# Optimization experiments

Hardware: AMD Instinct MI355X
Metric: run time of the kernel (lower is better)

The kernel has to match this reference:

```python
import jax, jax.numpy as jnp
import numpy as np

B, T, C = 2, 2048, 1024
NH = 16
HD = C // NH  # 64
FF = 4 * C
EPS = 1e-5


def layer_norm(x, w, b):
    mu = jnp.mean(x, axis=-1, keepdims=True)
    var = jnp.mean(jnp.square(x - mu), axis=-1, keepdims=True)
    return (x - mu) * jax.lax.rsqrt(var + EPS) * w + b


def setup_inputs() -> dict:
    key = jax.random.key(0)
    ks = jax.random.split(key, 12)
    s_in = 1.0 / np.sqrt(C)
    s_ff = 1.0 / np.sqrt(FF)
    return {
        "x": jax.random.normal(ks[0], (B, T, C), jnp.float32),
        "ln1_w": jnp.ones((C,), jnp.float32),
        "ln1_b": jnp.zeros((C,), jnp.float32),
        "Wq": jax.random.normal(ks[1], (C, C), jnp.float32) * s_in,
        "Wk": jax.random.normal(ks[2], (C, C), jnp.float32) * s_in,
        "Wv": jax.random.normal(ks[3], (C, C), jnp.float32) * s_in,
        "Wp": jax.random.normal(ks[4], (C, C), jnp.float32) * s_in,
        "bp": jnp.zeros((C,), jnp.float32),
        "ln2_w": jnp.ones((C,), jnp.float32),
        "ln2_b": jnp.zeros((C,), jnp.float32),
        "W1": jax.random.normal(ks[5], (C, FF), jnp.float32) * s_in,
        "b1": jnp.zeros((FF,), jnp.float32),
        "W2": jax.random.normal(ks[6], (FF, C), jnp.float32) * s_ff,
        "b2": jnp.zeros((C,), jnp.float32),
    }


def reference(x, ln1_w, ln1_b, Wq, Wk, Wv, Wp, bp, ln2_w, ln2_b, W1, b1, W2, b2):
    scale = HD ** (-0.5)
    h = layer_norm(x, ln1_w, ln1_b)  # [B,T,C]
    # project and split heads: [B,T,NH,HD] -> [B,NH,T,HD]
    q = (h @ Wq).reshape(B, T, NH, HD).transpose(0, 2, 1, 3)
    k = (h @ Wk).reshape(B, T, NH, HD).transpose(0, 2, 1, 3)
    v = (h @ Wv).reshape(B, T, NH, HD).transpose(0, 2, 1, 3)
    scores = jnp.einsum("bhqd,bhkd->bhqk", q, k) * scale  # [B,NH,T,T]
    causal = jnp.tril(jnp.ones((T, T), jnp.bool_))
    scores = jnp.where(causal, scores, -jnp.inf)
    attn = jax.nn.softmax(scores, axis=-1)
    o = jnp.einsum("bhqk,bhkd->bhqd", attn, v)  # [B,NH,T,HD]
    o = o.transpose(0, 2, 1, 3).reshape(B, T, C)
    x = x + o @ Wp + bp
    h2 = layer_norm(x, ln2_w, ln2_b)
    x = x + jax.nn.relu(h2 @ W1 + b1) @ W2 + b2
    return x
```

## Files before the change

### kernel.cpp

```cpp
#include <hip/hip_runtime.h>
#include <hip/hip_bf16.h>

using u16 = unsigned short;
typedef short v8s __attribute__((ext_vector_type(8)));
typedef float v4f __attribute__((ext_vector_type(4)));

#define B_ 2
#define T_ 2048
#define C_ 1024
#define NH_ 16
#define HD_ 64
#define FF_ 4096
#define NT (B_*T_)
#define QKVC 3072

__device__ __forceinline__ u16 f2b(float f) {
  union { float f; unsigned int i; } v; v.f = f;
  unsigned int r = (v.i + 0x7FFFu + ((v.i >> 16) & 1u)) >> 16;
  return (u16)r;
}
__device__ __forceinline__ v4f mfma16(v8s a, v8s b, v4f c) {
  return __builtin_amdgcn_mfma_f32_16x16x32_bf16(a, b, c, 0, 0, 0);
}
__device__ __forceinline__ void glds16(const u16* g, u16* l) {
  __builtin_amdgcn_global_load_lds(
      (const __attribute__((address_space(1))) unsigned int*)g,
      (__attribute__((address_space(3))) unsigned int*)l, 16, 0, 0);
}

__global__ __launch_bounds__(256) void wcvt_kernel(const float* __restrict__ W,
    u16* __restrict__ Wt, int K, int N) {
  __shared__ float t[32][33];
  int tx = threadIdx.x & 31, ty = threadIdx.x >> 5;
  int n0 = blockIdx.x * 32, k0 = blockIdx.y * 32;
#pragma unroll
  for (int j = 0; j < 4; ++j)
    t[ty + j * 8][tx] = W[(size_t)(k0 + ty + j * 8) * N + n0 + tx];
  __syncthreads();
#pragma unroll
  for (int j = 0; j < 4; ++j)
    Wt[(size_t)(n0 + ty + j * 8) * K + k0 + tx] = f2b(t[tx][ty + j * 8]);
}

__global__ __launch_bounds__(256) void ln_kernel(const float* __restrict__ x,
    const float* __restrict__ w, const float* __restrict__ b, u16* __restrict__ y) {
  int row = blockIdx.x;
  int tid = threadIdx.x;
  const float* xr = x + (size_t)row * C_;
  float4 f4 = *(const float4*)&xr[tid * 4];
  float f[4] = {f4.x, f4.y, f4.z, f4.w};
  float s1 = 0.f, s2 = 0.f;
#pragma unroll
  for (int i = 0; i < 4; ++i) { s1 += f[i]; s2 += f[i] * f[i]; }
#pragma unroll
  for (int off = 32; off > 0; off >>= 1) {
    s1 += __shfl_down(s1, off);
    s2 += __shfl_down(s2, off);
  }
  __shared__ float red[10];
  int lane = tid & 63, wid = tid >> 6;
  if (lane == 0) { red[wid] = s1; red[4 + wid] = s2; }
  __syncthreads();
  if (tid == 0) {
    float a = red[0] + red[1] + red[2] + red[3];
    float q = red[4] + red[5] + red[6] + red[7];
    float mu = a * (1.f / C_);
    float var = q * (1.f / C_) - mu * mu;
    red[8] = mu; red[9] = rsqrtf(var + 1e-5f);
  }
  __syncthreads();
  float mu = red[8], rs = red[9];
  union { uint2 v; u16 s[4]; } st;
#pragma unroll
  for (int i = 0; i < 4; ++i) {
    int c = tid * 4 + i;
    st.s[i] = f2b((f[i] - mu) * rs * w[c] + b[c]);
  }
  *(uint2*)&y[(size_t)row * C_ + tid * 4] = st.v;
}

__global__ __launch_bounds__(256) void gemm_bt(const u16* __restrict__ X,
    const u16* __restrict__ Wt, const float* __restrict__ bias,
    const float* __restrict__ resf, u16* __restrict__ Yb, float* __restrict__ Yf,
    float* __restrict__ Yfz1, int M, int N, int lda, int ldb, int kspl, int relu) {
  __shared__ __align__(16) u16 As[2][128 * 32];
  __shared__ __align__(16) u16 Bs[2][128 * 32];
  int tid = threadIdx.x, lane = tid & 63, w = tid >> 6;
  int wm = w >> 1, wn = w & 1, quad = lane >> 4, lcol = lane & 15;
  int m0 = blockIdx.y * 128, n0 = blockIdx.x * 128;
  int koff = blockIdx.z * kspl;
  v4f acc[4][4] = {};
  int sr = lane >> 2, sc = lane & 3;
  const u16* gA = X  + (size_t)(m0 + w * 32 + sr) * lda + koff + sc * 8;
  const u16* gB = Wt + (size_t)(n0 + w * 32 + sr) * ldb + koff + sc * 8;
  u16* lA0 = As[0] + (w * 32) * 32;
  u16* lA1 = As[1] + (w * 32) * 32;
  u16* lB0 = Bs[0] + (w * 32) * 32;
  u16* lB1 = Bs[1] + (w * 32) * 32;
  for (int k0 = 0; k0 < kspl; k0 += 64) {
    __syncthreads();
    glds16(gA + k0,                        lA0);
    glds16(gA + k0 + (size_t)16 * lda,     lA0 + 16 * 32);
    glds16(gA + k0 + 32,                   lA1);
    glds16(gA + k0 + 32 + (size_t)16 * lda, lA1 + 16 * 32);
    glds16(gB + k0,                        lB0);
    glds16(gB + k0 + (size_t)16 * ldb,     lB0 + 16 * 32);
    glds16(gB + k0 + 32,                   lB1);
    glds16(gB + k0 + 32 + (size_t)16 * ldb, lB1 + 16 * 32);
    __syncthreads();
#pragma unroll
    for (int kh = 0; kh < 2; ++kh) {
      v8s a[4], b[4];
#pragma unroll
      for (int i = 0; i < 4; ++i) {
        a[i] = *(v8s*)&As[kh][(wm * 64 + i * 16 + lcol) * 32 + quad * 8];
        b[i] = *(v8s*)&Bs[kh][(wn * 64 + i * 16 + lcol) * 32 + quad * 8];
      }
#pragma unroll
      for (int i = 0; i < 4; ++i)
#pragma unroll
        for (int j = 0; j < 4; ++j)
          acc[i][j] = mfma16(a[i], b[j], acc[i][j]);
    }
  }
  float* yf = blockIdx.z ? Yfz1 : Yf;
#pragma unroll
  for (int i = 0; i < 4; ++i) {
    int mb = m0 + wm * 64 + i * 16 + quad * 4;
#pragma unroll
    for (int j = 0; j < 4; ++j) {
      int n = n0 + wn * 64 + j * 16 + lcol;
#pragma unroll
      for (int r = 0; r < 4; ++r) {
        float v = acc[i][j][r];
        if (bias) v += bias[n];
        if (resf) v += resf[(size_t)(mb + r) * N + n];
        if (relu) v = fmaxf(v, 0.f);
        if (Yb) Yb[(size_t)(mb + r) * N + n] = f2b(v);
        else    yf[(size_t)(mb + r) * N + n] = v;
      }
    }
  }
}

__global__ __launch_bounds__(256) void gemm_bt_n64(const u16* __restrict__ X,
    const u16* __restrict__ Wt, const float* __restrict__ bias,
    const float* __restrict__ resf, u16* __restrict__ Yb, float* __restrict__ Yf,
    int M, int N, int K, int relu) {
  __shared__ __align__(16) u16 As[128 * 32];
  __shared__ __align__(16) u16 Bs[64 * 32];
  int tid = threadIdx.x, lane = tid & 63, w = tid >> 6;
  int wm = w >> 1, wn = w & 1, quad = lane >> 4, lcol = lane & 15;
  int m0 = blockIdx.y * 128, n0 = blockIdx.x * 64;
  v4f acc[4][2] = {};
  int sr = lane >> 2, sc = lane & 3;
  const u16* gA = X  + (size_t)(m0 + w * 32 + sr) * K + sc * 8;
  const u16* gB = Wt + (size_t)(n0 + w * 16 + sr) * K + sc * 8;
  u16* lA = As + (w * 32) * 32;
  u16* lB = Bs + (w * 16) * 32;
  for (int k0 = 0; k0 < K; k0 += 32) {
    __syncthreads();
    glds16(gA + k0, lA);
    glds16(gA + k0 + (size_t)16 * K, lA + 16 * 32);
    glds16(gB + k0, lB);
    __syncthreads();
    v8s a[4], b[2];
#pragma unroll
    for (int i = 0; i < 4; ++i)
      a[i] = *(v8s*)&As[(wm * 64 + i * 16 + lcol) * 32 + quad * 8];
#pragma unroll
    for (int j = 0; j < 2; ++j)
      b[j] = *(v8s*)&Bs[(wn * 32 + j * 16 + lcol) * 32 + quad * 8];
#pragma unroll
    for (int i = 0; i < 4; ++i)
#pragma unroll
      for (int j = 0; j < 2; ++j)
        acc[i][j] = mfma16(a[i], b[j], acc[i][j]);
  }
#pragma unroll
  for (int i = 0; i < 4; ++i) {
    int mb = m0 + wm * 64 + i * 16 + quad * 4;
#pragma unroll
    for (int j = 0; j < 2; ++j) {
      int n = n0 + wn * 32 + j * 16 + lcol;
#pragma unroll
      for (int r = 0; r < 4; ++r) {
        float v = acc[i][j][r];
        if (bias) v += bias[n];
        if (resf) v += resf[(size_t)(mb + r) * N + n];
        if (relu) v = fmaxf(v, 0.f);
        if (Yb) Yb[(size_t)(mb + r) * N + n] = f2b(v);
        else    Yf[(size_t)(mb + r) * N + n] = v;
      }
    }
  }
}

__global__ __launch_bounds__(256) void add4_kernel(float* __restrict__ out,
    const float* __restrict__ p0, const float* __restrict__ bias,
    const float* __restrict__ res) {
  size_t e0 = ((size_t)blockIdx.x * 256 + threadIdx.x) * 4;
  int col = (int)(e0 & (C_ - 1));
  float4 o = *(float4*)&out[e0];
  float4 p = *(const float4*)&p0[e0];
  float4 r = *(const float4*)&res[e0];
  float4 bb = *(const float4*)&bias[col];
  o.x += p.x + r.x + bb.x;
  o.y += p.y + r.y + bb.y;
  o.z += p.z + r.z + bb.z;
  o.w += p.w + r.w + bb.w;
  *(float4*)&out[e0] = o;
}

__global__ __launch_bounds__(256) void vt_kernel(const u16* __restrict__ QKV,
    u16* __restrict__ VT) {
  int bh = blockIdx.x, tt = blockIdx.y;
  int b = bh >> 4, h = bh & 15;
  int tid = threadIdx.x;
  __shared__ u16 L[64 * 72];
  int r = tid >> 2, g = tid & 3;
  size_t row = ((size_t)(b * T_ + tt * 64 + r)) * QKVC + 2 * C_ + h * HD_;
  union { uint4 v; u16 s[8]; } a0, a1;
  a0.v = *(const uint4*)&QKV[row + g * 8];
  a1.v = *(const uint4*)&QKV[row + 32 + g * 8];
#pragma unroll
  for (int e = 0; e < 8; ++e) L[(g * 8 + e) * 72 + r] = a0.s[e];
#pragma unroll
  for (int e = 0; e < 8; ++e) L[(32 + g * 8 + e) * 72 + r] = a1.s[e];
  __syncthreads();
  size_t orow = ((size_t)(bh * 64 + r)) * T_ + tt * 64;
  *(uint4*)&VT[orow + g * 8]      = *(uint4*)&L[r * 72 + g * 8];
  *(uint4*)&VT[orow + 32 + g * 8] = *(uint4*)&L[r * 72 + 32 + g * 8];
}

__global__ __launch_bounds__(256) void attn_kernel(const u16* __restrict__ QKV,
    const u16* __restrict__ VT, u16* __restrict__ Ob) {
  int bh = blockIdx.x, y = blockIdx.y;
  int b = bh >> 4, h = bh & 15;
  int tid = threadIdx.x, lane = tid & 63, wid = tid >> 6;
  int quad = lane >> 4, lcol = lane & 15;
  __shared__ __align__(16) u16 Ps[4][32 * 72];
  const float SC = 0.125f * 1.44269504f;
  const float EB = 8.0f * 1.44269504f;
  const u16* kbase = QKV + (size_t)b * T_ * QKVC + C_ + h * HD_;
  const u16* vbase = VT + (size_t)(bh * 64) * T_;
  u16* psw = Ps[wid];

  auto ldk = [&](v8s (&ak)[4][2], int kb) {
#pragma unroll
    for (int cg = 0; cg < 4; ++cg)
#pragma unroll
      for (int kh = 0; kh < 2; ++kh)
        ak[cg][kh] = *(const v8s*)&kbase[(size_t)(kb * 64 + cg * 16 + lcol) * QKVC + kh * 32 + quad * 8];
  };

#pragma unroll
  for (int pi = 0; pi < 2; ++pi) {
    int qt = pi ? (15 - y) : y;
    int qg[2];
    v8s bq[2][2];
#pragma unroll
    for (int j = 0; j < 2; ++j) {
      qg[j] = qt * 128 + wid * 32 + j * 16 + lcol;
#pragma unroll
      for (int kh = 0; kh < 2; ++kh)
        bq[j][kh] = *(const v8s*)&QKV[(size_t)(b * T_ + qg[j]) * QKVC + h * HD_ + kh * 32 + quad * 8];
    }
    float l_i[2] = {0.f, 0.f};
    v4f accO[4][2] = {};
    int kbmax = 2 * qt + (wid >> 1);

    auto ctile = [&](v8s (&ak)[4][2], int kb, bool diag) {
      v8s av[4][2];
#pragma unroll
      for (int df = 0; df < 4; ++df)
#pragma unroll
        for (int kh = 0; kh < 2; ++kh)
          av[df][kh] = *(const v8s*)&vbase[(size_t)(df * 16 + lcol) * T_ + kb * 64 + kh * 32 + quad * 8];
#pragma unroll
      for (int j = 0; j < 2; ++j) {
        v4f s[4];
#pragma unroll
        for (int cg = 0; cg < 4; ++cg) {
          v4f acc = {};
          acc = mfma16(ak[cg][1], bq[j][1], acc);
          s[cg] = mfma16(ak[cg][0], bq[j][0], acc);
        }
        float ps = 0.f;
#pragma unroll
        for (int cg = 0; cg < 4; ++cg) {
          union { u16 s4[4]; unsigned long long ll; } pk;
#pragma unroll
          for (int rg = 0; rg < 4; ++rg) {
            float pv = exp2f(s[cg][rg] * SC - EB);
            if (diag) {
              int kt = kb * 64 + cg * 16 + quad * 4 + rg;
              pv = (kt <= qg[j]) ? pv : 0.f;
            }
            ps += pv;
            pk.s4[rg] = f2b(pv);
          }
          *(unsigned long long*)&psw[(j * 16 + lcol) * 72 + cg * 16 + quad * 4] = pk.ll;
        }
        ps += __shfl_xor(ps, 16);
        ps += __shfl_xor(ps, 32);
        l_i[j] += ps;
        v8s bp0 = *(v8s*)&psw[(j * 16 + lcol) * 72 + quad * 8];
        v8s bp1 = *(v8s*)&psw[(j * 16 + lcol) * 72 + 32 + quad * 8];
#pragma unroll
        for (int df = 0; df < 4; ++df) {
          v4f t = mfma16(av[df][1], bp1, accO[df][j]);
          accO[df][j] = mfma16(av[df][0], bp0, t);
        }
      }
    };

    v8s a0k[4][2], a1k[4][2];
    ldk(a0k, 0);
    for (int kb = 0; kb <= kbmax; kb += 2) {
      if (kb + 1 <= kbmax) ldk(a1k, kb + 1);
      ctile(a0k, kb, kb == kbmax);
      if (kb + 1 <= kbmax) {
        if (kb + 2 <= kbmax) ldk(a0k, kb + 2);
        ctile(a1k, kb + 1, (kb + 1) == kbmax);
      }
    }
#pragma unroll
    for (int j = 0; j < 2; ++j) {
      float inv = 1.f / l_i[j];
      size_t orow = ((size_t)(b * T_ + qg[j])) * C_ + h * HD_;
#pragma unroll
      for (int df = 0; df < 4; ++df) {
        union { u16 s4[4]; unsigned long long ll; } ok;
#pragma unroll
        for (int rg = 0; rg < 4; ++rg) ok.s4[rg] = f2b(accO[df][j][rg] * inv);
        *(unsigned long long*)&Ob[orow + df * 16 + quad * 4] = ok.ll;
      }
    }
  }
}

extern "C" void kernel_launch(void* const* d_in, const int* in_sizes, int n_in,
                              void* d_out, int out_size, void* d_ws, size_t ws_size,
                              hipStream_t stream) {
  (void)in_sizes; (void)n_in; (void)out_size; (void)ws_size;
  const float* x    = (const float*)d_in[0];
  const float* ln1w = (const float*)d_in[1];
  const float* ln1b = (const float*)d_in[2];
  const float* Wq   = (const float*)d_in[3];
  const float* Wk   = (const float*)d_in[4];
  const float* Wv   = (const float*)d_in[5];
  const float* Wp   = (const float*)d_in[6];
  const float* bp   = (const float*)d_in[7];
  const float* ln2w = (const float*)d_in[8];
  const float* ln2b = (const float*)d_in[9];
  const float* W1   = (const float*)d_in[10];
  const float* b1   = (const float*)d_in[11];
  const float* W2   = (const float*)d_in[12];
  const float* b2   = (const float*)d_in[13];
  float* out = (float*)d_out;
  char* ws = (char*)d_ws;
  const size_t MB = 1024 * 1024;
  u16*   h1    = (u16*)(ws);
  u16*   VT    = (u16*)(ws);
  u16*   QKVb  = (u16*)(ws + 8  * MB);
  u16*   Ob    = (u16*)(ws + 32 * MB);
  float* xa    = (float*)(ws + 40 * MB);
  u16*   h2    = (u16*)(ws);
  u16*   f1    = (u16*)(ws + 8 * MB);
  u16*   Wqkvt = (u16*)(ws + 56 * MB);
  u16*   Wpt   = (u16*)(ws + 62 * MB);
  u16*   W1t   = (u16*)(ws + 64 * MB);
  u16*   W2t   = (u16*)(ws + 72 * MB);
  float* p0    = (float*)(ws + 56 * MB);

  wcvt_kernel<<<dim3(32, 32),  256, 0, stream>>>(Wq, Wqkvt,                1024, 1024);
  wcvt_kernel<<<dim3(32, 32),  256, 0, stream>>>(Wk, Wqkvt + 1024 * 1024,  1024, 1024);
  wcvt_kernel<<<dim3(32, 32),  256, 0, stream>>>(Wv, Wqkvt + 2048 * 1024,  1024, 1024);
  wcvt_kernel<<<dim3(32, 32),  256, 0, stream>>>(Wp, Wpt,                  1024, 1024);
  wcvt_kernel<<<dim3(128, 32), 256, 0, stream>>>(W1, W1t,                  1024, 4096);
  wcvt_kernel<<<dim3(32, 128), 256, 0, stream>>>(W2, W2t,                  4096, 1024);

  ln_kernel<<<NT, 256, 0, stream>>>(x, ln1w, ln1b, h1);
  gemm_bt<<<dim3(QKVC / 128, NT / 128, 1), 256, 0, stream>>>(
      h1, Wqkvt, nullptr, nullptr, QKVb, nullptr, nullptr, NT, QKVC, C_, C_, C_, 0);
  vt_kernel<<<dim3(B_ * NH_, T_ / 64), 256, 0, stream>>>(QKVb, VT);
  attn_kernel<<<dim3(B_ * NH_, T_ / 256), 256, 0, stream>>>(QKVb, VT, Ob);
  gemm_bt_n64<<<dim3(C_ / 64, NT / 128), 256, 0, stream>>>(
      Ob, Wpt, bp, x, nullptr, xa, NT, C_, C_, 0);
  ln_kernel<<<NT, 256, 0, stream>>>(xa, ln2w, ln2b, h2);
  gemm_bt<<<dim3(FF_ / 128, NT / 128, 1), 256, 0, stream>>>(
      h2, W1t, b1, nullptr, f1, nullptr, nullptr, NT, FF_, C_, C_, C_, 1);
  gemm_bt<<<dim3(C_ / 128, NT / 128, 2), 256, 0, stream>>>(
      f1, W2t, nullptr, nullptr, nullptr, p0, out, NT, C_, FF_, FF_, FF_ / 2, 0);
  add4_kernel<<<(NT * C_) / (256 * 4), 256, 0, stream>>>(out, p0, b2, xa);
}
```

Measured before the change: 445.9 us.

## Halve attention query tile per block and deepen projection GEMM K-step

The attention kernel now gives each wave 16 query rows instead of 32, with 64-row query tiles per block and twice as many blocks, still paired so the causal work stays balanced. This is meant to raise occupancy and parallelism and to trim per-wave registers. The trade-off is that each loaded K/V tile is reused across fewer queries. Separately, the N=64 projection GEMM now loads 64 K elements per sync instead of 32, halving barriers at the cost of more shared memory.

```diff
diff --git a/kernel.cpp b/kernel.cpp
--- a/kernel.cpp
+++ b/kernel.cpp
@@ -147,8 +147,8 @@
     const u16* __restrict__ Wt, const float* __restrict__ bias,
     const float* __restrict__ resf, u16* __restrict__ Yb, float* __restrict__ Yf,
     int M, int N, int K, int relu) {
-  __shared__ __align__(16) u16 As[128 * 32];
-  __shared__ __align__(16) u16 Bs[64 * 32];
+  __shared__ __align__(16) u16 As[2][128 * 32];
+  __shared__ __align__(16) u16 Bs[2][64 * 32];
   int tid = threadIdx.x, lane = tid & 63, w = tid >> 6;
   int wm = w >> 1, wn = w & 1, quad = lane >> 4, lcol = lane & 15;
   int m0 = blockIdx.y * 128, n0 = blockIdx.x * 64;
@@ -156,26 +156,34 @@
   int sr = lane >> 2, sc = lane & 3;
   const u16* gA = X  + (size_t)(m0 + w * 32 + sr) * K + sc * 8;
   const u16* gB = Wt + (size_t)(n0 + w * 16 + sr) * K + sc * 8;
-  u16* lA = As + (w * 32) * 32;
-  u16* lB = Bs + (w * 16) * 32;
-  for (int k0 = 0; k0 < K; k0 += 32) {
+  u16* lA0 = As[0] + (w * 32) * 32;
+  u16* lA1 = As[1] + (w * 32) * 32;
+  u16* lB0 = Bs[0] + (w * 16) * 32;
+  u16* lB1 = Bs[1] + (w * 16) * 32;
+  for (int k0 = 0; k0 < K; k0 += 64) {
     __syncthreads();
-    glds16(gA + k0, lA);
-    glds16(gA + k0 + (size_t)16 * K, lA + 16 * 32);
-    glds16(gB + k0, lB);
+    glds16(gA + k0,                       lA0);
+    glds16(gA + k0 + (size_t)16 * K,      lA0 + 16 * 32);
+    glds16(gA + k0 + 32,                  lA1);
+    glds16(gA + k0 + 32 + (size_t)16 * K, lA1 + 16 * 32);
+    glds16(gB + k0,                       lB0);
+    glds16(gB + k0 + 32,                  lB1);
     __syncthreads();
-    v8s a[4], b[2];
-#pragma unroll
-    for (int i = 0; i < 4; ++i)
-      a[i] = *(v8s*)&As[(wm * 64 + i * 16 + lcol) * 32 + quad * 8];
-#pragma unroll
-    for (int j = 0; j < 2; ++j)
-      b[j] = *(v8s*)&Bs[(wn * 32 + j * 16 + lcol) * 32 + quad * 8];
-#pragma unroll
-    for (int i = 0; i < 4; ++i)
+#pragma unroll
+    for (int kh = 0; kh < 2; ++kh) {
+      v8s a[4], b[2];
+#pragma unroll
+      for (int i = 0; i < 4; ++i)
+        a[i] = *(v8s*)&As[kh][(wm * 64 + i * 16 + lcol) * 32 + quad * 8];
 #pragma unroll
       for (int j = 0; j < 2; ++j)
-        acc[i][j] = mfma16(a[i], b[j], acc[i][j]);
+        b[j] = *(v8s*)&Bs[kh][(wn * 32 + j * 16 + lcol) * 32 + quad * 8];
+#pragma unroll
+      for (int i = 0; i < 4; ++i)
+#pragma unroll
+        for (int j = 0; j < 2; ++j)
+          acc[i][j] = mfma16(a[i], b[j], acc[i][j]);
+    }
   }
 #pragma unroll
   for (int i = 0; i < 4; ++i) {
@@ -239,7 +247,7 @@
   int b = bh >> 4, h = bh & 15;
   int tid = threadIdx.x, lane = tid & 63, wid = tid >> 6;
   int quad = lane >> 4, lcol = lane & 15;
-  __shared__ __align__(16) u16 Ps[4][32 * 72];
+  __shared__ __align__(16) u16 Ps[4][16 * 72];
   const float SC = 0.125f * 1.44269504f;
   const float EB = 8.0f * 1.44269504f;
   const u16* kbase = QKV + (size_t)b * T_ * QKVC + C_ + h * HD_;
@@ -256,19 +264,15 @@
 
 #pragma unroll
   for (int pi = 0; pi < 2; ++pi) {
-    int qt = pi ? (15 - y) : y;
-    int qg[2];
-    v8s bq[2][2];
-#pragma unroll
-    for (int j = 0; j < 2; ++j) {
-      qg[j] = qt * 128 + wid * 32 + j * 16 + lcol;
-#pragma unroll
-      for (int kh = 0; kh < 2; ++kh)
-        bq[j][kh] = *(const v8s*)&QKV[(size_t)(b * T_ + qg[j]) * QKVC + h * HD_ + kh * 32 + quad * 8];
-    }
-    float l_i[2] = {0.f, 0.f};
-    v4f accO[4][2] = {};
-    int kbmax = 2 * qt + (wid >> 1);
+    int qt = pi ? (31 - y) : y;
+    int qg = qt * 64 + wid * 16 + lcol;
+    v8s bq[2];
+#pragma unroll
+    for (int kh = 0; kh < 2; ++kh)
+      bq[kh] = *(const v8s*)&QKV[(size_t)(b * T_ + qg) * QKVC + h * HD_ + kh * 32 + quad * 8];
+    float l_i = 0.f;
+    v4f accO[4] = {};
+    int kbmax = qt;
 
     auto ctile = [&](v8s (&ak)[4][2], int kb, bool diag) {
       v8s av[4][2];
@@ -277,41 +281,38 @@
 #pragma unroll
         for (int kh = 0; kh < 2; ++kh)
           av[df][kh] = *(const v8s*)&vbase[(size_t)(df * 16 + lcol) * T_ + kb * 64 + kh * 32 + quad * 8];
-#pragma unroll
-      for (int j = 0; j < 2; ++j) {
-        v4f s[4];
-#pragma unroll
-        for (int cg = 0; cg < 4; ++cg) {
-          v4f acc = {};
-          acc = mfma16(ak[cg][1], bq[j][1], acc);
-          s[cg] = mfma16(ak[cg][0], bq[j][0], acc);
+      v4f s[4];
+#pragma unroll
+      for (int cg = 0; cg < 4; ++cg) {
+        v4f acc = {};
+        acc = mfma16(ak[cg][1], bq[1], acc);
+        s[cg] = mfma16(ak[cg][0], bq[0], acc);
+      }
+      float ps = 0.f;
+#pragma unroll
+      for (int cg = 0; cg < 4; ++cg) {
+        union { u16 s4[4]; unsigned long long ll; } pk;
+#pragma unroll
+        for (int rg = 0; rg < 4; ++rg) {
+          float pv = exp2f(s[cg][rg] * SC - EB);
+          if (diag) {
+            int kt = kb * 64 + cg * 16 + quad * 4 + rg;
+            pv = (kt <= qg) ? pv : 0.f;
+          }
+          ps += pv;
+          pk.s4[rg] = f2b(pv);
         }
-        float ps = 0.f;
-#pragma unroll
-        for (int cg = 0; cg < 4; ++cg) {
-          union { u16 s4[4]; unsigned long long ll; } pk;
-#pragma unroll
-          for (int rg = 0; rg < 4; ++rg) {
-            float pv = exp2f(s[cg][rg] * SC - EB);
-            if (diag) {
-              int kt = kb * 64 + cg * 16 + quad * 4 + rg;
-              pv = (kt <= qg[j]) ? pv : 0.f;
-            }
-            ps += pv;
-            pk.s4[rg] = f2b(pv);
-          }
-          *(unsigned long long*)&psw[(j * 16 + lcol) * 72 + cg * 16 + quad * 4] = pk.ll;
-        }
-        ps += __shfl_xor(ps, 16);
-        ps += __shfl_xor(ps, 32);
-        l_i[j] += ps;
-        v8s bp0 = *(v8s*)&psw[(j * 16 + lcol) * 72 + quad * 8];
-        v8s bp1 = *(v8s*)&psw[(j * 16 + lcol) * 72 + 32 + quad * 8];
-#pragma unroll
-        for (int df = 0; df < 4; ++df) {
-          v4f t = mfma16(av[df][1], bp1, accO[df][j]);
-          accO[df][j] = mfma16(av[df][0], bp0, t);
-        }
+        *(unsigned long long*)&psw[lcol * 72 + cg * 16 + quad * 4] = pk.ll;
+      }
+      ps += __shfl_xor(ps, 16);
+      ps += __shfl_xor(ps, 32);
+      l_i += ps;
+      v8s bp0 = *(v8s*)&psw[lcol * 72 + quad * 8];
+      v8s bp1 = *(v8s*)&psw[lcol * 72 + 32 + quad * 8];
+#pragma unroll
+      for (int df = 0; df < 4; ++df) {
+        v4f t = mfma16(av[df][1], bp1, accO[df]);
+        accO[df] = mfma16(av[df][0], bp0, t);
       }
     };
 
@@ -325,17 +326,14 @@
         ctile(a1k, kb + 1, (kb + 1) == kbmax);
       }
     }
-#pragma unroll
-    for (int j = 0; j < 2; ++j) {
-      float inv = 1.f / l_i[j];
-      size_t orow = ((size_t)(b * T_ + qg[j])) * C_ + h * HD_;
-#pragma unroll
-      for (int df = 0; df < 4; ++df) {
-        union { u16 s4[4]; unsigned long long ll; } ok;
-#pragma unroll
-        for (int rg = 0; rg < 4; ++rg) ok.s4[rg] = f2b(accO[df][j][rg] * inv);
-        *(unsigned long long*)&Ob[orow + df * 16 + quad * 4] = ok.ll;
-      }
+    float inv = 1.f / l_i;
+    size_t orow = ((size_t)(b * T_ + qg)) * C_ + h * HD_;
+#pragma unroll
+    for (int df = 0; df < 4; ++df) {
+      union { u16 s4[4]; unsigned long long ll; } ok;
+#pragma unroll
+      for (int rg = 0; rg < 4; ++rg) ok.s4[rg] = f2b(accO[df][rg] * inv);
+      *(unsigned long long*)&Ob[orow + df * 16 + quad * 4] = ok.ll;
     }
   }
 }
@@ -385,7 +383,7 @@
   gemm_bt<<<dim3(QKVC / 128, NT / 128, 1), 256, 0, stream>>>(
       h1, Wqkvt, nullptr, nullptr, QKVb, nullptr, nullptr, NT, QKVC, C_, C_, C_, 0);
   vt_kernel<<<dim3(B_ * NH_, T_ / 64), 256, 0, stream>>>(QKVb, VT);
-  attn_kernel<<<dim3(B_ * NH_, T_ / 256), 256, 0, stream>>>(QKVb, VT, Ob);
+  attn_kernel<<<dim3(B_ * NH_, T_ / 128), 256, 0, stream>>>(QKVb, VT, Ob);
   gemm_bt_n64<<<dim3(C_ / 64, NT / 128), 256, 0, stream>>>(
       Ob, Wpt, bp, x, nullptr, xa, NT, C_, C_, 0);
   ln_kernel<<<NT, 256, 0, stream>>>(xa, ln2w, ln2b, h2);
```

Measured after the change: 479.0 us. 1.07x slower.

## Split attention key range across two blocks and merge partials; deepen out-proj K-step

Applied to the files above, without the earlier changes.

The attention kernel gets a third grid dimension of 2. Each block handles one half of the causal key range and writes a bf16 partial output plus its softmax denominator. A new reduction kernel combines the two halves, weighting each by its share of the denominator. This is valid because the softmax uses a fixed exponent bias rather than a running max, and it doubles the block count so the attention grid better fills the GPU. It costs extra bf16 rounding and extra global traffic for the partials. Separately, the n64 projection GEMM now loads 64 K elements per sync, halving the number of barriers.

```diff
diff --git a/kernel.cpp b/kernel.cpp
--- a/kernel.cpp
+++ b/kernel.cpp
@@ -18,6 +18,9 @@
   union { float f; unsigned int i; } v; v.f = f;
   unsigned int r = (v.i + 0x7FFFu + ((v.i >> 16) & 1u)) >> 16;
   return (u16)r;
+}
+__device__ __forceinline__ float b2f(u16 u) {
+  union { unsigned int i; float f; } v; v.i = ((unsigned int)u) << 16; return v.f;
 }
 __device__ __forceinline__ v4f mfma16(v8s a, v8s b, v4f c) {
   return __builtin_amdgcn_mfma_f32_16x16x32_bf16(a, b, c, 0, 0, 0);
@@ -147,8 +150,8 @@
     const u16* __restrict__ Wt, const float* __restrict__ bias,
     const float* __restrict__ resf, u16* __restrict__ Yb, float* __restrict__ Yf,
     int M, int N, int K, int relu) {
-  __shared__ __align__(16) u16 As[128 * 32];
-  __shared__ __align__(16) u16 Bs[64 * 32];
+  __shared__ __align__(16) u16 As[2][128 * 32];
+  __shared__ __align__(16) u16 Bs[2][64 * 32];
   int tid = threadIdx.x, lane = tid & 63, w = tid >> 6;
   int wm = w >> 1, wn = w & 1, quad = lane >> 4, lcol = lane & 15;
   int m0 = blockIdx.y * 128, n0 = blockIdx.x * 64;
@@ -156,26 +159,34 @@
   int sr = lane >> 2, sc = lane & 3;
   const u16* gA = X  + (size_t)(m0 + w * 32 + sr) * K + sc * 8;
   const u16* gB = Wt + (size_t)(n0 + w * 16 + sr) * K + sc * 8;
-  u16* lA = As + (w * 32) * 32;
-  u16* lB = Bs + (w * 16) * 32;
-  for (int k0 = 0; k0 < K; k0 += 32) {
+  u16* lA0 = As[0] + (w * 32) * 32;
+  u16* lA1 = As[1] + (w * 32) * 32;
+  u16* lB0 = Bs[0] + (w * 16) * 32;
+  u16* lB1 = Bs[1] + (w * 16) * 32;
+  for (int k0 = 0; k0 < K; k0 += 64) {
     __syncthreads();
-    glds16(gA + k0, lA);
-    glds16(gA + k0 + (size_t)16 * K, lA + 16 * 32);
-    glds16(gB + k0, lB);
+    glds16(gA + k0,                       lA0);
+    glds16(gA + k0 + (size_t)16 * K,      lA0 + 16 * 32);
+    glds16(gA + k0 + 32,                  lA1);
+    glds16(gA + k0 + 32 + (size_t)16 * K, lA1 + 16 * 32);
+    glds16(gB + k0,                       lB0);
+    glds16(gB + k0 + 32,                  lB1);
     __syncthreads();
-    v8s a[4], b[2];
-#pragma unroll
-    for (int i = 0; i < 4; ++i)
-      a[i] = *(v8s*)&As[(wm * 64 + i * 16 + lcol) * 32 + quad * 8];
-#pragma unroll
-    for (int j = 0; j < 2; ++j)
-      b[j] = *(v8s*)&Bs[(wn * 32 + j * 16 + lcol) * 32 + quad * 8];
-#pragma unroll
-    for (int i = 0; i < 4; ++i)
+#pragma unroll
+    for (int kh = 0; kh < 2; ++kh) {
+      v8s a[4], b[2];
+#pragma unroll
+      for (int i = 0; i < 4; ++i)
+        a[i] = *(v8s*)&As[kh][(wm * 64 + i * 16 + lcol) * 32 + quad * 8];
 #pragma unroll
       for (int j = 0; j < 2; ++j)
-        acc[i][j] = mfma16(a[i], b[j], acc[i][j]);
+        b[j] = *(v8s*)&Bs[kh][(wn * 32 + j * 16 + lcol) * 32 + quad * 8];
+#pragma unroll
+      for (int i = 0; i < 4; ++i)
+#pragma unroll
+        for (int j = 0; j < 2; ++j)
+          acc[i][j] = mfma16(a[i], b[j], acc[i][j]);
+    }
   }
 #pragma unroll
   for (int i = 0; i < 4; ++i) {
@@ -234,8 +245,8 @@
 }
 
 __global__ __launch_bounds__(256) void attn_kernel(const u16* __restrict__ QKV,
-    const u16* __restrict__ VT, u16* __restrict__ Ob) {
-  int bh = blockIdx.x, y = blockIdx.y;
+    const u16* __restrict__ VT, u16* __restrict__ Opart, float* __restrict__ lpart) {
+  int bh = blockIdx.x, y = blockIdx.y, z = blockIdx.z;
   int b = bh >> 4, h = bh & 15;
   int tid = threadIdx.x, lane = tid & 63, wid = tid >> 6;
   int quad = lane >> 4, lcol = lane & 15;
@@ -245,6 +256,8 @@
   const u16* kbase = QKV + (size_t)b * T_ * QKVC + C_ + h * HD_;
   const u16* vbase = VT + (size_t)(bh * 64) * T_;
   u16* psw = Ps[wid];
+  u16* Os = Opart + (size_t)z * NT * C_;
+  float* ls = lpart + (size_t)z * 32 * T_;
 
   auto ldk = [&](v8s (&ak)[4][2], int kb) {
 #pragma unroll
@@ -269,6 +282,9 @@
     float l_i[2] = {0.f, 0.f};
     v4f accO[4][2] = {};
     int kbmax = 2 * qt + (wid >> 1);
+    int mid = (kbmax + 2) >> 1;
+    int lo = z ? mid : 0;
+    int hi = z ? kbmax : (mid - 1);
 
     auto ctile = [&](v8s (&ak)[4][2], int kb, bool diag) {
       v8s av[4][2];
@@ -315,29 +331,52 @@
       }
     };
 
-    v8s a0k[4][2], a1k[4][2];
-    ldk(a0k, 0);
-    for (int kb = 0; kb <= kbmax; kb += 2) {
-      if (kb + 1 <= kbmax) ldk(a1k, kb + 1);
-      ctile(a0k, kb, kb == kbmax);
-      if (kb + 1 <= kbmax) {
-        if (kb + 2 <= kbmax) ldk(a0k, kb + 2);
-        ctile(a1k, kb + 1, (kb + 1) == kbmax);
+    if (lo <= hi) {
+      v8s a0k[4][2], a1k[4][2];
+      ldk(a0k, lo);
+      for (int kb = lo; kb <= hi; kb += 2) {
+        if (kb + 1 <= hi) ldk(a1k, kb + 1);
+        ctile(a0k, kb, kb == kbmax);
+        if (kb + 1 <= hi) {
+          if (kb + 2 <= hi) ldk(a0k, kb + 2);
+          ctile(a1k, kb + 1, (kb + 1) == kbmax);
+        }
       }
     }
 #pragma unroll
     for (int j = 0; j < 2; ++j) {
-      float inv = 1.f / l_i[j];
+      float inv = (l_i[j] > 0.f) ? (1.f / l_i[j]) : 0.f;
       size_t orow = ((size_t)(b * T_ + qg[j])) * C_ + h * HD_;
+      if (quad == 0) ls[bh * T_ + qg[j]] = l_i[j];
 #pragma unroll
       for (int df = 0; df < 4; ++df) {
         union { u16 s4[4]; unsigned long long ll; } ok;
 #pragma unroll
         for (int rg = 0; rg < 4; ++rg) ok.s4[rg] = f2b(accO[df][j][rg] * inv);
-        *(unsigned long long*)&Ob[orow + df * 16 + quad * 4] = ok.ll;
-      }
-    }
-  }
+        *(unsigned long long*)&Os[orow + df * 16 + quad * 4] = ok.ll;
+      }
+    }
+  }
+}
+
+__global__ __launch_bounds__(256) void ared_kernel(const u16* __restrict__ Opart,
+    const float* __restrict__ lpart, u16* __restrict__ Ob) {
+  size_t e0 = ((size_t)blockIdx.x * 256 + threadIdx.x) * 4;
+  int tb = (int)(e0 >> 10);
+  int col = (int)(e0 & (C_ - 1));
+  int bq = tb >> 11, t = tb & (T_ - 1);
+  int h = col >> 6;
+  int lidx = (bq * 16 + h) * T_ + t;
+  float l0 = lpart[lidx], l1 = lpart[32 * T_ + lidx];
+  float inv = 1.f / (l0 + l1);
+  float w0 = l0 * inv, w1 = l1 * inv;
+  union { uint2 v; u16 s[4]; } a, b, o;
+  a.v = *(const uint2*)&Opart[e0];
+  b.v = *(const uint2*)&Opart[(size_t)NT * C_ + e0];
+#pragma unroll
+  for (int i = 0; i < 4; ++i)
+    o.s[i] = f2b(b2f(a.s[i]) * w0 + b2f(b.s[i]) * w1);
+  *(uint2*)&Ob[e0] = o.v;
 }
 
 extern "C" void kernel_launch(void* const* d_in, const int* in_sizes, int n_in,
@@ -366,9 +405,11 @@
   u16*   QKVb  = (u16*)(ws + 8  * MB);
   u16*   Ob    = (u16*)(ws + 32 * MB);
   float* xa    = (float*)(ws + 40 * MB);
+  u16*   Opart = (u16*)(ws + 40 * MB);
   u16*   h2    = (u16*)(ws);
   u16*   f1    = (u16*)(ws + 8 * MB);
   u16*   Wqkvt = (u16*)(ws + 56 * MB);
+  float* lpart = (float*)(ws + 56 * MB);
   u16*   Wpt   = (u16*)(ws + 62 * MB);
   u16*   W1t   = (u16*)(ws + 64 * MB);
   u16*   W2t   = (u16*)(ws + 72 * MB);
@@ -385,7 +426,8 @@
   gemm_bt<<<dim3(QKVC / 128, NT / 128, 1), 256, 0, stream>>>(
       h1, Wqkvt, nullptr, nullptr, QKVb, nullptr, nullptr, NT, QKVC, C_, C_, C_, 0);
   vt_kernel<<<dim3(B_ * NH_, T_ / 64), 256, 0, stream>>>(QKVb, VT);
-  attn_kernel<<<dim3(B_ * NH_, T_ / 256), 256, 0, stream>>>(QKVb, VT, Ob);
+  attn_kernel<<<dim3(B_ * NH_, T_ / 256, 2), 256, 0, stream>>>(QKVb, VT, Opart, lpart);
+  ared_kernel<<<(NT * C_) / (256 * 4), 256, 0, stream>>>(Opart, lpart, Ob);
   gemm_bt_n64<<<dim3(C_ / 64, NT / 128), 256, 0, stream>>>(
       Ob, Wpt, bp, x, nullptr, xa, NT, C_, C_, 0);
   ln_kernel<<<NT, 256, 0, stream>>>(xa, ln2w, ln2b, h2);
```

Measured after the change: 448.0 us. About the same (+0.5%).
